# Optimization experiments

Measured on AMD Instinct MI355X. Metric: run time of the kernel, lower is better.

The kernel has to match this reference:

```python
import jax, jax.numpy as jnp
import numpy as np

H = 8          # num_heads
NEG = -1e30    # masked-score value
EPS = 1e-5


def layer_norm(h, g, b):
    mu = jnp.mean(h, -1, keepdims=True)
    v = jnp.mean(jnp.square(h - mu), -1, keepdims=True)
    return (h - mu) * jax.lax.rsqrt(v + EPS) * g + b


def mha(q_in, kv_in, in_w, in_b, out_w, out_b, mask):
    # in_w: [3D, D] packed q/k/v projections (PyTorch MultiheadAttention layout)
    D = q_in.shape[-1]
    dh = D // H
    wq, wk, wv = in_w[:D], in_w[D:2 * D], in_w[2 * D:]
    bq, bk, bv = in_b[:D], in_b[D:2 * D], in_b[2 * D:]
    q = (q_in @ wq.T + bq).reshape(q_in.shape[0], q_in.shape[1], H, dh)
    k = (kv_in @ wk.T + bk).reshape(kv_in.shape[0], kv_in.shape[1], H, dh)
    v = (kv_in @ wv.T + bv).reshape(kv_in.shape[0], kv_in.shape[1], H, dh)
    s = jnp.einsum('bqhd,bkhd->bhqk', q, k) / jnp.sqrt(jnp.float32(dh))
    if mask is not None:
        s = s + mask  # [1,1,S,S] additive causal mask
    a = jax.nn.softmax(s, axis=-1)
    o = jnp.einsum('bhqk,bkhd->bqhd', a, v).reshape(q_in.shape[0], q_in.shape[1], D)
    return o @ out_w.T + out_b


def _forward(x, start_query, one_emb, zero_emb,
             sa_in_w, sa_in_b, sa_out_w, sa_out_b,
             ca_in_w, ca_in_b, ca_out_w, ca_out_b,
             lin1_w, lin1_b, lin2_w, lin2_b,
             ln_g, ln_b, cls_w, cls_b, label):
    B, S, D = x.shape
    n = label.shape[0]  # == S
    # Teacher-forced decoder inputs: [start_query, emb(label[0]), ..., emb(label[n-2])]
    tok = jnp.where((label[:-1] > 0.5)[:, None], one_emb[None, :], zero_emb[None, :])  # [n-1, D]
    tgt = jnp.concatenate([start_query[None, :], tok], axis=0)  # [n, D]
    h = jnp.broadcast_to(tgt[None], (B, n, D))
    causal = jnp.tril(jnp.ones((n, n), dtype=bool))
    mask = jnp.where(causal, 0.0, NEG).astype(x.dtype)[None, None]
    L = sa_in_w.shape[0]
    for l in range(L):
        # post-LN TransformerDecoderLayer (PyTorch default, relu FFN)
        sa = mha(h, h, sa_in_w[l], sa_in_b[l], sa_out_w[l], sa_out_b[l], mask)
        h = layer_norm(h + sa, ln_g[l, 0], ln_b[l, 0])
        ca = mha(h, x, ca_in_w[l], ca_in_b[l], ca_out_w[l], ca_out_b[l], None)
        h = layer_norm(h + ca, ln_g[l, 1], ln_b[l, 1])
        ff = jax.nn.relu(h @ lin1_w[l].T + lin1_b[l]) @ lin2_w[l].T + lin2_b[l]
        h = layer_norm(h + ff, ln_g[l, 2], ln_b[l, 2])
    # classifier + sigmoid; output[b, i] == decoder(tf[:1+i])[-1] of the original loop
    return jax.nn.sigmoid(h @ cls_w.T + cls_b)  # [B, n, 1]


def setup_inputs() -> dict:
    key = jax.random.key(0)
    ks = iter(jax.random.split(key, 32))
    B, S, D, FF, L = 8, 1024, 1024, 2048, 6

    def w(shape, s=0.02):
        return jax.random.normal(next(ks), shape, jnp.float32) * s

    return dict(
        x=jax.random.normal(next(ks), (B, S, D), jnp.float32),
        label=jax.random.uniform(next(ks), (S,), jnp.float32),
        start_query=jax.random.uniform(next(ks), (D,), jnp.float32),
        one_emb=jax.random.uniform(next(ks), (D,), jnp.float32),
        zero_emb=jax.random.uniform(next(ks), (D,), jnp.float32),
        sa_in_w=w((L, 3 * D, D)), sa_in_b=jnp.zeros((L, 3 * D), jnp.float32),
        sa_out_w=w((L, D, D)), sa_out_b=jnp.zeros((L, D), jnp.float32),
        ca_in_w=w((L, 3 * D, D)), ca_in_b=jnp.zeros((L, 3 * D), jnp.float32),
        ca_out_w=w((L, D, D)), ca_out_b=jnp.zeros((L, D), jnp.float32),
        lin1_w=w((L, FF, D)), lin1_b=jnp.zeros((L, FF), jnp.float32),
        lin2_w=w((L, D, FF)), lin2_b=jnp.zeros((L, D), jnp.float32),
        ln_g=jnp.ones((L, 3, D), jnp.float32), ln_b=jnp.zeros((L, 3, D), jnp.float32),
        cls_w=w((1, D)), cls_b=jnp.zeros((1,), jnp.float32),
    )


def reference(x, label, start_query, one_emb, zero_emb,
              sa_in_w, sa_in_b, sa_out_w, sa_out_b,
              ca_in_w, ca_in_b, ca_out_w, ca_out_b,
              lin1_w, lin1_b, lin2_w, lin2_b,
              ln_g, ln_b, cls_w, cls_b):
    return _forward(x, start_query, one_emb, zero_emb,
                    sa_in_w, sa_in_b, sa_out_w, sa_out_b,
                    ca_in_w, ca_in_b, ca_out_w, ca_out_b,
                    lin1_w, lin1_b, lin2_w, lin2_b,
                    ln_g, ln_b, cls_w, cls_b, label)
```

## Files before the change

kernel.cpp:

```cpp
#include <hip/hip_runtime.h>
#include <stdint.h>

typedef __attribute__((ext_vector_type(8))) short short8;
typedef __attribute__((ext_vector_type(4))) float f32x4;
typedef __attribute__((ext_vector_type(4))) float float4v;
typedef __attribute__((ext_vector_type(4))) unsigned short ushort4v;

__device__ __forceinline__ float b2f(short u) {
  union { float f; uint32_t i; } v; v.i = ((uint32_t)(unsigned short)u) << 16; return v.f;
}
__device__ __forceinline__ short f2b(float f) {
  uint32_t x = __float_as_uint(f);
  uint32_t r = (x + 0x7fffu + ((x >> 16) & 1u)) >> 16;
  return (short)r;
}
__device__ __forceinline__ void gload16(const short* g, short* l) {
  __builtin_amdgcn_global_load_lds((__attribute__((address_space(1))) const void*)g,
                                   (__attribute__((address_space(3))) void*)l, 16, 0, 0);
}

__global__ void f2b_kernel(const float* __restrict__ in, short* __restrict__ out, int n4) {
  int i = blockIdx.x * blockDim.x + threadIdx.x;
  int stride = gridDim.x * blockDim.x;
  for (; i < n4; i += stride) {
// ... 25 lines not shown
  const int w3 = w & 3;
  const int rlo = lane >> 3;
  const int us = (lane & 7) ^ rlo;
#pragma unroll
  for (int q = 0; q < 4; ++q) {
    int c;
    if (w < 4) c = g2 * 8 + w3 * 2 + (q & 1) + (q >> 1) * 16;
    else       c = g2 * 4 + w3 + (q & 1) * 8 + (q >> 1) * 16;
    int rih = (c & 15) * 8 + rlo;
    gload16(mat + (rc0 + (c >> 4) * 128 + rih) * (size_t)K + kt * 64 + us * 8,
            dstbuf + ((w >> 2) * 32 + c) * 512);
  }
}

template <int EPI>
__global__ __launch_bounds__(512, 2) void gemm256(const short* __restrict__ A,
                                                  const short* __restrict__ W,
                                                  const float* __restrict__ bias,
                                                  short* __restrict__ C,
                                                  int M, int N, int K) {
  __shared__ short lds[2 * 4 * 8192];
  const int tid = threadIdx.x, lane = tid & 63, w = tid >> 6;
  const int g = lane >> 4, l15 = lane & 15;
  const int wm = w >> 2, wn = w & 3;
  const int nbx = N >> 8;
  int nwg = gridDim.x, orig = blockIdx.x, cpx = nwg >> 3;
  int id = (orig & 7) * cpx + (orig >> 3);
  int bx = id % nbx, by = id / nbx;
  const size_t rowA = (size_t)by * 256, colB = (size_t)bx * 256;
  const int NT = K >> 6;

  const short* smat = (w < 4) ? A : W;
  const size_t src0 = (w < 4) ? rowA : colB;

  f32x4 acc[8][4];
#pragma unroll
  for (int i = 0; i < 8; ++i)
#pragma unroll
    for (int j = 0; j < 4; ++j) acc[i][j] = (f32x4){0.f, 0.f, 0.f, 0.f};

  int sxz0 = g ^ (l15 & 7);
  int sxz1 = (4 + g) ^ (l15 & 7);
  const short* abase = lds + wm * 8192 + l15 * 64;
  const short* bbase = lds + (2 + (wn >> 1)) * 8192 + ((wn & 1) * 64 + l15) * 64;

  stage_grp(smat, src0, K, 0, lds, w, lane, 0);
  stage_grp(smat, src0, K, 0, lds, w, lane, 1);
  asm volatile("s_waitcnt vmcnt(0)" ::: "memory");
  __builtin_amdgcn_s_barrier();

  int p = 0;
  for (int t = 0; t < NT; ++t) {
    const int po = p * 32768;
    short* nbuf = lds + (p ^ 1) * 32768;
    if (t + 1 < NT) stage_grp(smat, src0, K, t + 1, nbuf, w, lane, 0);
    short8 af[4][2], bf0[2][2], bf1[2][2];

#pragma unroll
    for (int i = 0; i < 4; ++i) {
      af[i][0] = *(const short8*)(abase + po + i * 1024 + sxz0 * 8);
      af[i][1] = *(const short8*)(abase + po + i * 1024 + sxz1 * 8);
    }
#pragma unroll
    for (int j = 0; j < 2; ++j) {
      bf0[j][0] = *(const short8*)(bbase + po + j * 1024 + sxz0 * 8);
      bf0[j][1] = *(const short8*)(bbase + po + j * 1024 + sxz1 * 8);
    }
    __builtin_amdgcn_s_barrier();
    __builtin_amdgcn_s_setprio(1);
#pragma unroll
    for (int i = 0; i < 4; ++i)
#pragma unroll
      for (int j = 0; j < 2; ++j)
#pragma unroll
        for (int ks = 0; ks < 2; ++ks)
          acc[i][j] = __builtin_amdgcn_mfma_f32_16x16x32_bf16(af[i][ks], bf0[j][ks], acc[i][j], 0, 0, 0);
    __builtin_amdgcn_s_setprio(0);
    if (t + 1 < NT) {
      asm volatile("s_waitcnt vmcnt(4)" ::: "memory");
      stage_grp(smat, src0, K, t + 1, nbuf, w, lane, 1);
    } else {
      asm volatile("s_waitcnt vmcnt(0)" ::: "memory");
    }
    __builtin_amdgcn_s_barrier();

#pragma unroll
    for (int j = 0; j < 2; ++j) {
      bf1[j][0] = *(const short8*)(bbase + po + (2 + j) * 1024 + sxz0 * 8);
      bf1[j][1] = *(const short8*)(bbase + po + (2 + j) * 1024 + sxz1 * 8);
    }
    __builtin_amdgcn_s_barrier();
    __builtin_amdgcn_s_setprio(1);
#pragma unroll
    for (int i = 0; i < 4; ++i)
#pragma unroll
      for (int j = 0; j < 2; ++j)
#pragma unroll
        for (int ks = 0; ks < 2; ++ks)
          acc[i][2 + j] = __builtin_amdgcn_mfma_f32_16x16x32_bf16(af[i][ks], bf1[j][ks], acc[i][2 + j], 0, 0, 0);
    __builtin_amdgcn_s_setprio(0);
    __builtin_amdgcn_s_barrier();

#pragma unroll
    for (int i = 0; i < 4; ++i) {
      af[i][0] = *(const short8*)(abase + po + (64 + i * 16) * 64 + sxz0 * 8);
      af[i][1] = *(const short8*)(abase + po + (64 + i * 16) * 64 + sxz1 * 8);
    }
    __builtin_amdgcn_s_barrier();
    __builtin_amdgcn_s_setprio(1);
#pragma unroll
    for (int i = 0; i < 4; ++i)
#pragma unroll
      for (int j = 0; j < 2; ++j)
#pragma unroll
        for (int ks = 0; ks < 2; ++ks)
          acc[4 + i][2 + j] = __builtin_amdgcn_mfma_f32_16x16x32_bf16(af[i][ks], bf1[j][ks], acc[4 + i][2 + j], 0, 0, 0);
    __builtin_amdgcn_s_setprio(0);
    __builtin_amdgcn_s_barrier();

    __builtin_amdgcn_s_setprio(1);
#pragma unroll
    for (int i = 0; i < 4; ++i)
#pragma unroll
      for (int j = 0; j < 2; ++j)
#pragma unroll
        for (int ks = 0; ks < 2; ++ks)
          acc[4 + i][j] = __builtin_amdgcn_mfma_f32_16x16x32_bf16(af[i][ks], bf0[j][ks], acc[4 + i][j], 0, 0, 0);
    __builtin_amdgcn_s_setprio(0);

    asm volatile("s_waitcnt vmcnt(4)" ::: "memory");
    __builtin_amdgcn_s_barrier();
    p ^= 1;
  }

  float bv[4];
#pragma unroll
  for (int j = 0; j < 4; ++j) bv[j] = bias[colB + wn * 64 + j * 16 + l15];
#pragma unroll
  for (int i = 0; i < 8; ++i) {
    size_t row = rowA + wm * 128 + i * 16 + g * 4;
#pragma unroll
    for (int j = 0; j < 4; ++j) {
      size_t col = colB + wn * 64 + j * 16 + l15;
#pragma unroll
      for (int r = 0; r < 4; ++r) {
        float v = acc[i][j][r] + bv[j];
        if (EPI == 1) v = fmaxf(v, 0.f);
        C[(row + r) * N + col] = f2b(v);
      }
    }
  }
}

__device__ __forceinline__ void stage_n128(const short* __restrict__ A, const short* __restrict__ W,
                                           size_t rowA, size_t colB, int K, int kt,
                                           short* dstbuf, int w, int lane, int grp) {
  const int rlo = lane >> 3;
  const int us = (lane & 7) ^ rlo;
  const int coff = kt * 64 + us * 8;
  if (grp == 0) {
#pragma unroll
    for (int q = 0; q < 4; ++q) {
      int c = w * 4 + q;
      gload16(A + (rowA + (c >> 4) * 128 + (c & 15) * 8 + rlo) * (size_t)K + coff,
              dstbuf + (c >> 4) * 8192 + (c & 15) * 512 + lane * 8);
    }
    int bc = (w & 3) + (w >> 2) * 8;
    gload16(W + (colB + bc * 8 + rlo) * (size_t)K + coff, dstbuf + 16384 + bc * 512 + lane * 8);
  } else {
    int bc = (w & 3) + (w >> 2) * 8 + 4;
    gload16(W + (colB + bc * 8 + rlo) * (size_t)K + coff, dstbuf + 16384 + bc * 512 + lane * 8);
  }
}

template <int EPI>
__global__ __launch_bounds__(512, 2) void gemm_n128(const short* __restrict__ A,
                                                    const short* __restrict__ W,
                                                    const float* __restrict__ bias,
                                                    short* __restrict__ C,
                                                    int M, int N, int K) {
  __shared__ short lds[2 * 24576];
  const int tid = threadIdx.x, lane = tid & 63, w = tid >> 6;
  const int g = lane >> 4, l15 = lane & 15;
  const int wm = w >> 1, wn = w & 1;
  const int nbx = N >> 7;
  int nwg = gridDim.x, orig = blockIdx.x, cpx = nwg >> 3;
  int id = (orig & 7) * cpx + (orig >> 3);
  int bx = id % nbx, by = id / nbx;
  const size_t rowA = (size_t)by * 256, colB = (size_t)bx * 128;
  const int NT = K >> 6;

  f32x4 acc[4][4];
#pragma unroll
  for (int i = 0; i < 4; ++i)
#pragma unroll
    for (int j = 0; j < 4; ++j) acc[i][j] = (f32x4){0.f, 0.f, 0.f, 0.f};

  const int sxz0 = g ^ (l15 & 7), sxz1 = (4 + g) ^ (l15 & 7);
  int aoff[4];
#pragma unroll
  for (int i = 0; i < 4; ++i) {
    int ra = wm * 64 + i * 16 + l15;
    aoff[i] = (ra >> 7) * 8192 + (ra & 127) * 64;
  }
  const int boffb = 16384 + (wn * 64 + l15) * 64;

  stage_n128(A, W, rowA, colB, K, 0, lds, w, lane, 0);
  stage_n128(A, W, rowA, colB, K, 0, lds, w, lane, 1);
  asm volatile("s_waitcnt vmcnt(0)" ::: "memory");
  __builtin_amdgcn_s_barrier();

  int p = 0;
  for (int t = 0; t < NT; ++t) {
    short* nbuf = lds + (p ^ 1) * 24576;
    if (t + 1 < NT) stage_n128(A, W, rowA, colB, K, t + 1, nbuf, w, lane, 0);
    const int po = p * 24576;
    short8 af[4][2], bf[2][2];
#pragma unroll
    for (int i = 0; i < 4; ++i) {
      af[i][0] = *(const short8*)(lds + po + aoff[i] + sxz0 * 8);
      af[i][1] = *(const short8*)(lds + po + aoff[i] + sxz1 * 8);
    }
#pragma unroll
    for (int j = 0; j < 2; ++j) {
      bf[j][0] = *(const short8*)(lds + po + boffb + j * 1024 + sxz0 * 8);
      bf[j][1] = *(const short8*)(lds + po + boffb + j * 1024 + sxz1 * 8);
    }
    __builtin_amdgcn_s_setprio(1);
#pragma unroll
    for (int i = 0; i < 4; ++i)
#pragma unroll
      for (int j = 0; j < 2; ++j)
#pragma unroll
        for (int ks = 0; ks < 2; ++ks)
          acc[i][j] = __builtin_amdgcn_mfma_f32_16x16x32_bf16(af[i][ks], bf[j][ks], acc[i][j], 0, 0, 0);
    __builtin_amdgcn_s_setprio(0);
    if (t + 1 < NT) {
      asm volatile("s_waitcnt vmcnt(5)" ::: "memory");
      stage_n128(A, W, rowA, colB, K, t + 1, nbuf, w, lane, 1);
    } else {
      asm volatile("s_waitcnt vmcnt(0)" ::: "memory");
    }
    __builtin_amdgcn_s_barrier();
#pragma unroll
    for (int j = 0; j < 2; ++j) {
      bf[j][0] = *(const short8*)(lds + po + boffb + 2048 + j * 1024 + sxz0 * 8);
      bf[j][1] = *(const short8*)(lds + po + boffb + 2048 + j * 1024 + sxz1 * 8);
    }
    __builtin_amdgcn_s_setprio(1);
#pragma unroll
    for (int i = 0; i < 4; ++i)
#pragma unroll
      for (int j = 0; j < 2; ++j)
#pragma unroll
        for (int ks = 0; ks < 2; ++ks)
          acc[i][2 + j] = __builtin_amdgcn_mfma_f32_16x16x32_bf16(af[i][ks], bf[j][ks], acc[i][2 + j], 0, 0, 0);
    __builtin_amdgcn_s_setprio(0);
    asm volatile("s_waitcnt vmcnt(1)" ::: "memory");
    __builtin_amdgcn_s_barrier();
    p ^= 1;
  }

  float bv[4];
#pragma unroll
  for (int j = 0; j < 4; ++j) bv[j] = bias[colB + wn * 64 + j * 16 + l15];
#pragma unroll
  for (int i = 0; i < 4; ++i) {
    size_t row = rowA + wm * 64 + i * 16 + g * 4;
#pragma unroll
    for (int j = 0; j < 4; ++j) {
      size_t col = colB + wn * 64 + j * 16 + l15;
#pragma unroll
      for (int r = 0; r < 4; ++r) {
        float v = acc[i][j][r] + bv[j];
        if (EPI == 1) v = fmaxf(v, 0.f);
        C[(row + r) * N + col] = f2b(v);
      }
    }
  }
}

__global__ __launch_bounds__(256) void tv_kernel(const short* __restrict__ src, int ld, int voff,
                                                 short* __restrict__ vt) {
  __shared__ short t[64 * 72];
  const int kt = blockIdx.x * 64, dt = blockIdx.y * 64, bh = blockIdx.z;
  const int b = bh >> 3, hh = bh & 7;
  const short* s = src + (size_t)(b * 1024 + kt) * ld + voff + hh * 128 + dt;
#pragma unroll
  for (int p = 0; p < 2; ++p) {
    int idx = p * 256 + threadIdx.x;
    int r = idx >> 3, u = idx & 7;
    *(short8*)&t[r * 72 + u * 8] = *(const short8*)&s[(size_t)r * ld + u * 8];
  }
  __syncthreads();
#pragma unroll
  for (int p = 0; p < 2; ++p) {
    int idx = p * 256 + threadIdx.x;
    int dd = idx >> 3, u = idx & 7;
    short8 o;
#pragma unroll
    for (int j = 0; j < 8; ++j) o[j] = t[(u * 8 + j) * 72 + dd];
    *(short8*)&vt[((size_t)bh * 128 + dt + dd) * 1024 + kt + u * 8] = o;
  }
}

template <bool CAUSAL>
__global__ __launch_bounds__(256, 2) void attn_kernel(const short* __restrict__ Qb, int ldq, int qoff,
                                                      const short* __restrict__ Kb, int ldk, int koff,
                                                      const short* __restrict__ Vt,
                                                      short* __restrict__ Ob) {
  __shared__ short k_lds[64 * 128];
  __shared__ short v_lds[128 * 64];
  __shared__ short p_lds[4 * 32 * 72];
  const int tid = threadIdx.x, lane = tid & 63, w = tid >> 6;
  const int g = lane >> 4, l15 = lane & 15;
  const int bh = blockIdx.y, b = bh >> 3, hh = bh & 7;
  int qi = blockIdx.x;
  if (CAUSAL) qi = (blockIdx.y & 32) ? 7 - qi : qi;
  const int q0 = qi * 128;
  const float scale = 0.08838834764831845f;
  const int ntiles = CAUSAL ? (q0 >> 6) + 2 : 16;

  const int kr = (w * 4) * 4 + (lane >> 4);
  const int vd = (w * 4) * 8 + (lane >> 3);

  short8 qf[2][4];
#pragma unroll
  for (int fm = 0; fm < 2; ++fm) {
    int row = q0 + w * 32 + fm * 16 + l15;
    const short* qp = Qb + (size_t)(b * 1024 + row) * ldq + qoff + hh * 128;
#pragma unroll
    for (int t = 0; t < 4; ++t) qf[fm][t] = *(const short8*)(qp + t * 32 + g * 8);
  }

  f32x4 oacc[2][8];
  f32x4 lacc[2];
  float m_st[2][4];
#pragma unroll
  for (int fm = 0; fm < 2; ++fm) {
#pragma unroll
    for (int fo = 0; fo < 8; ++fo) oacc[fm][fo] = (f32x4){0.f, 0.f, 0.f, 0.f};
    lacc[fm] = (f32x4){0.f, 0.f, 0.f, 0.f};
#pragma unroll
    for (int r = 0; r < 4; ++r) m_st[fm][r] = -3.0e38f;
  }
  const short8 ones = {16256, 16256, 16256, 16256, 16256, 16256, 16256, 16256};

#pragma unroll
  for (int c = 0; c < 4; ++c) {
    int ch = w * 4 + c;
    int r = kr + c * 4;
    int us = (lane & 15) ^ (r & 7);
    gload16(Kb + (size_t)(b * 1024 + r) * ldk + koff + hh * 128 + us * 8, k_lds + ch * 512);
    int d = vd + c * 8;
    int usv = (lane & 7) ^ (d & 7);
    gload16(Vt + ((size_t)bh * 128 + d) * 1024 + usv * 8, v_lds + ch * 512);
  }
  __builtin_amdgcn_sched_barrier(0);
  short8 kreg[4], vreg[4];
  if (ntiles > 1) {
#pragma unroll
    for (int c = 0; c < 4; ++c) {
      int r = kr + c * 4;
      int us = (lane & 15) ^ (r & 7);
      kreg[c] = *(const short8*)(Kb + (size_t)(b * 1024 + 64 + r) * ldk + koff + hh * 128 + us * 8);
      int d = vd + c * 8;
      int usv = (lane & 7) ^ (d & 7);
      vreg[c] = *(const short8*)(Vt + ((size_t)bh * 128 + d) * 1024 + 64 + usv * 8);
    }
    asm volatile("s_waitcnt vmcnt(8)" ::: "memory");
  } else {
    asm volatile("s_waitcnt vmcnt(0)" ::: "memory");
  }
  __builtin_amdgcn_s_barrier();

  for (int kt = 0; kt < ntiles; ++kt) {
    f32x4 sacc[2][4];
#pragma unroll
    for (int fm = 0; fm < 2; ++fm)
#pragma unroll
      for (int fn = 0; fn < 4; ++fn) sacc[fm][fn] = (f32x4){0.f, 0.f, 0.f, 0.f};
#pragma unroll
    for (int t = 0; t < 4; ++t) {
      short8 kf[4];
#pragma unroll
      for (int fn = 0; fn < 4; ++fn) {
        int rowk = fn * 16 + l15;
        int u = (4 * t + g) ^ (rowk & 7);
        kf[fn] = *(const short8*)((const char*)k_lds + rowk * 256 + u * 16);
      }
      __builtin_amdgcn_s_setprio(1);
#pragma unroll
      for (int fm = 0; fm < 2; ++fm)
#pragma unroll
        for (int fn = 0; fn < 4; ++fn)
          sacc[fm][fn] = __builtin_amdgcn_mfma_f32_16x16x32_bf16(qf[fm][t], kf[fn], sacc[fm][fn], 0, 0, 0);
      __builtin_amdgcn_s_setprio(0);
    }

#pragma unroll
    for (int fm = 0; fm < 2; ++fm)
#pragma unroll
      for (int reg = 0; reg < 4; ++reg) {
        float sv[4];
        float mt = -3.0e38f;
#pragma unroll
        for (int fn = 0; fn < 4; ++fn) {
          float s = sacc[fm][fn][reg] * scale;
          if (CAUSAL) {
            int kg = kt * 64 + fn * 16 + l15;
            int qg = q0 + w * 32 + fm * 16 + g * 4 + reg;
            if (kg > qg) s = -1e30f;
          }
          sv[fn] = s;
          mt = fmaxf(mt, s);
        }
#pragma unroll
        for (int off = 1; off < 16; off <<= 1) mt = fmaxf(mt, __shfl_xor(mt, off));
        float mo = m_st[fm][reg];
        float mn = fmaxf(mo, mt);
        float corr = __expf(mo - mn);
#pragma unroll
        for (int fn = 0; fn < 4; ++fn) {
          float p = __expf(sv[fn] - mn);
          p_lds[w * 2304 + (fm * 16 + g * 4 + reg) * 72 + fn * 16 + l15] = f2b(p);
        }
        m_st[fm][reg] = mn;
        lacc[fm][reg] *= corr;
#pragma unroll
        for (int fo = 0; fo < 8; ++fo) oacc[fm][fo][reg] *= corr;
      }

#pragma unroll
    for (int t = 0; t < 2; ++t) {
      short8 pf[2];
#pragma unroll
      for (int fm = 0; fm < 2; ++fm)
        pf[fm] = *(const short8*)(p_lds + w * 2304 + (fm * 16 + l15) * 72 + t * 32 + g * 8);
      __builtin_amdgcn_s_setprio(1);
      lacc[0] = __builtin_amdgcn_mfma_f32_16x16x32_bf16(pf[0], ones, lacc[0], 0, 0, 0);
      lacc[1] = __builtin_amdgcn_mfma_f32_16x16x32_bf16(pf[1], ones, lacc[1], 0, 0, 0);
      __builtin_amdgcn_s_setprio(0);
#pragma unroll
      for (int fo = 0; fo < 8; ++fo) {
        int rowd = fo * 16 + l15;
        int u = (4 * t + g) ^ (rowd & 7);
        short8 vf = *(const short8*)((const char*)v_lds + rowd * 128 + u * 16);
        __builtin_amdgcn_s_setprio(1);
#pragma unroll
        for (int fm = 0; fm < 2; ++fm)
          oacc[fm][fo] = __builtin_amdgcn_mfma_f32_16x16x32_bf16(pf[fm], vf, oacc[fm][fo], 0, 0, 0);
        __builtin_amdgcn_s_setprio(0);
      }
    }

    if (kt + 1 < ntiles) {
      __builtin_amdgcn_s_barrier();
      asm volatile("s_waitcnt vmcnt(0)" ::: "memory");
#pragma unroll
      for (int c = 0; c < 4; ++c) {
        int ch = w * 4 + c;
        *(short8*)(k_lds + ch * 512 + lane * 8) = kreg[c];
        *(short8*)(v_lds + ch * 512 + lane * 8) = vreg[c];
      }
      if (kt + 2 < ntiles) {
#pragma unroll
        for (int c = 0; c < 4; ++c) {
          int r = kr + c * 4;
          int us = (lane & 15) ^ (r & 7);
          kreg[c] = *(const short8*)(Kb + (size_t)(b * 1024 + (kt + 2) * 64 + r) * ldk + koff + hh * 128 + us * 8);
          int d = vd + c * 8;
          int usv = (lane & 7) ^ (d & 7);
          vreg[c] = *(const short8*)(Vt + ((size_t)bh * 128 + d) * 1024 + (kt + 2) * 64 + usv * 8);
        }
      }
      asm volatile("s_waitcnt lgkmcnt(0)" ::: "memory");
      __builtin_amdgcn_s_barrier();
    }
  }

#pragma unroll
  for (int fm = 0; fm < 2; ++fm)
#pragma unroll
    for (int fo = 0; fo < 8; ++fo)
#pragma unroll
      for (int reg = 0; reg < 4; ++reg) {
        int row = q0 + w * 32 + fm * 16 + g * 4 + reg;
        int col = hh * 128 + fo * 16 + l15;
        float o = oacc[fm][fo][reg] / lacc[fm][reg];
        Ob[(size_t)(b * 1024 + row) * 1024 + col] = f2b(o);
      }
}

__global__ __launch_bounds__(128) void ln_kernel(const short* __restrict__ h,
                                                 const short* __restrict__ delta,
                                                 const float* __restrict__ gg,
                                                 const float* __restrict__ bb,
                                                 short* __restrict__ out) {
  __shared__ float red[4];
  const int row = blockIdx.x, tid = threadIdx.x;
  const short8 hv = *(const short8*)(h + (size_t)row * 1024 + tid * 8);
  const short8 dv = *(const short8*)(delta + (size_t)row * 1024 + tid * 8);
  float x[8];
  float s = 0.f, s2 = 0.f;
#pragma unroll
  for (int j = 0; j < 8; ++j) {
    x[j] = b2f(hv[j]) + b2f(dv[j]);
    s += x[j];
    s2 += x[j] * x[j];
  }
#pragma unroll
  for (int o = 1; o < 64; o <<= 1) { s += __shfl_xor(s, o); s2 += __shfl_xor(s2, o); }
  if ((tid & 63) == 0) { red[(tid >> 6) * 2] = s; red[(tid >> 6) * 2 + 1] = s2; }
  __syncthreads();
  s = red[0] + red[2];
  s2 = red[1] + red[3];
  const float mu = s * (1.f / 1024.f);
  const float var = s2 * (1.f / 1024.f) - mu * mu;
  const float rs = rsqrtf(var + 1e-5f);
  short8 o;
#pragma unroll
  for (int j = 0; j < 8; ++j) {
    int d = tid * 8 + j;
    o[j] = f2b((x[j] - mu) * rs * gg[d] + bb[d]);
  }
  *(short8*)(out + (size_t)row * 1024 + tid * 8) = o;
}

__global__ __launch_bounds__(256) void cls_kernel(const short* __restrict__ h,
                                                  const float* __restrict__ wv,
                                                  const float* __restrict__ bias,
                                                  float* __restrict__ out) {
  const int lane = threadIdx.x & 63, w = threadIdx.x >> 6;
  const int row = blockIdx.x * 4 + w;
  const short* hp = h + (size_t)row * 1024 + lane * 16;
  float sum = 0.f;
#pragma unroll
  for (int i = 0; i < 2; ++i) {
    short8 v = *(const short8*)(hp + i * 8);
#pragma unroll
    for (int j = 0; j < 8; ++j) sum += b2f(v[j]) * wv[lane * 16 + i * 8 + j];
  }
#pragma unroll
  for (int o = 1; o < 64; o <<= 1) sum += __shfl_xor(sum, o);
  if (lane == 0) {
    float z = sum + bias[0];
    out[row] = 1.f / (1.f + __expf(-z));
  }
}

#define O_SA_IN  ((size_t)0)
#define O_SA_OUT ((size_t)18874368)
#define O_CA_IN  ((size_t)25165824)
#define O_CA_OUT ((size_t)44040192)
#define O_LIN1   ((size_t)50331648)
#define O_LIN2   ((size_t)62914560)
#define O_X      ((size_t)75497472)
#define O_H      ((size_t)83886080)
#define O_QKV    ((size_t)92274688)
#define O_ATTN   ((size_t)117440512)
#define O_DELTA  ((size_t)125829120)
#define O_VT     ((size_t)134217728)
#define O_FF1    ((size_t)142606336)

extern "C" void kernel_launch(void* const* d_in, const int* in_sizes, int n_in,
                              void* d_out, int out_size, void* d_ws, size_t ws_size,
                              hipStream_t stream) {
  const float* x = (const float*)d_in[0];
  const float* label = (const float*)d_in[1];
  const float* sq = (const float*)d_in[2];
  const float* onee = (const float*)d_in[3];
  const float* zeroe = (const float*)d_in[4];
  const float* sa_in_w = (const float*)d_in[5];
  const float* sa_in_b = (const float*)d_in[6];
  const float* sa_out_w = (const float*)d_in[7];
  const float* sa_out_b = (const float*)d_in[8];
  const float* ca_in_w = (const float*)d_in[9];
  const float* ca_in_b = (const float*)d_in[10];
  const float* ca_out_w = (const float*)d_in[11];
  const float* ca_out_b = (const float*)d_in[12];
  const float* lin1_w = (const float*)d_in[13];
  const float* lin1_b = (const float*)d_in[14];
  const float* lin2_w = (const float*)d_in[15];
  const float* lin2_b = (const float*)d_in[16];
  const float* ln_g = (const float*)d_in[17];
  const float* ln_b = (const float*)d_in[18];
  const float* cls_w = (const float*)d_in[19];
  const float* cls_b = (const float*)d_in[20];

  short* ws = (short*)d_ws;
  short* w_sa_in = ws + O_SA_IN;
  short* w_sa_out = ws + O_SA_OUT;
  short* w_ca_in = ws + O_CA_IN;
  short* w_ca_out = ws + O_CA_OUT;
  short* w_lin1 = ws + O_LIN1;
  short* w_lin2 = ws + O_LIN2;
  short* xb = ws + O_X;
  short* hbuf = ws + O_H;
  short* qkv = ws + O_QKV;
  short* kvb = qkv + 8388608;
  short* attnb = ws + O_ATTN;
  short* delta = ws + O_DELTA;
  short* vt = ws + O_VT;
  short* ff1 = ws + O_FF1;

  f2b_kernel<<<4096, 256, 0, stream>>>(sa_in_w, w_sa_in, 18874368 / 4);
  f2b_kernel<<<4096, 256, 0, stream>>>(sa_out_w, w_sa_out, 6291456 / 4);
  f2b_kernel<<<4096, 256, 0, stream>>>(ca_in_w, w_ca_in, 18874368 / 4);
  f2b_kernel<<<4096, 256, 0, stream>>>(ca_out_w, w_ca_out, 6291456 / 4);
  f2b_kernel<<<4096, 256, 0, stream>>>(lin1_w, w_lin1, 12582912 / 4);
  f2b_kernel<<<4096, 256, 0, stream>>>(lin2_w, w_lin2, 12582912 / 4);
  f2b_kernel<<<4096, 256, 0, stream>>>(x, xb, 8388608 / 4);
  h0_kernel<<<1024, 256, 0, stream>>>(label, sq, onee, zeroe, hbuf);

  for (int l = 0; l < 6; ++l) {
    gemm256<0><<<384, 512, 0, stream>>>(hbuf, w_sa_in + (size_t)l * 3145728,
                                        sa_in_b + (size_t)l * 3072, qkv, 8192, 3072, 1024);
    tv_kernel<<<dim3(16, 2, 64), 256, 0, stream>>>(qkv, 3072, 2048, vt);
    attn_kernel<true><<<dim3(8, 64), 256, 0, stream>>>(qkv, 3072, 0, qkv, 3072, 1024, vt, attnb);
    gemm_n128<0><<<256, 512, 0, stream>>>(attnb, w_sa_out + (size_t)l * 1048576,
                                          sa_out_b + (size_t)l * 1024, delta, 8192, 1024, 1024);
    ln_kernel<<<8192, 128, 0, stream>>>(hbuf, delta, ln_g + (size_t)(l * 3 + 0) * 1024,
                                        ln_b + (size_t)(l * 3 + 0) * 1024, hbuf);
    gemm_n128<0><<<256, 512, 0, stream>>>(hbuf, w_ca_in + (size_t)l * 3145728,
                                          ca_in_b + (size_t)l * 3072, qkv, 8192, 1024, 1024);
    gemm256<0><<<256, 512, 0, stream>>>(xb, w_ca_in + (size_t)l * 3145728 + 1048576,
                                        ca_in_b + (size_t)l * 3072 + 1024, kvb, 8192, 2048, 1024);
    tv_kernel<<<dim3(16, 2, 64), 256, 0, stream>>>(kvb, 2048, 1024, vt);
    attn_kernel<false><<<dim3(8, 64), 256, 0, stream>>>(qkv, 1024, 0, kvb, 2048, 0, vt, attnb);
    gemm_n128<0><<<256, 512, 0, stream>>>(attnb, w_ca_out + (size_t)l * 1048576,
                                          ca_out_b + (size_t)l * 1024, delta, 8192, 1024, 1024);
    ln_kernel<<<8192, 128, 0, stream>>>(hbuf, delta, ln_g + (size_t)(l * 3 + 1) * 1024,
                                        ln_b + (size_t)(l * 3 + 1) * 1024, hbuf);
    gemm256<1><<<256, 512, 0, stream>>>(hbuf, w_lin1 + (size_t)l * 2097152,
                                        lin1_b + (size_t)l * 2048, ff1, 8192, 2048, 1024);
    gemm_n128<0><<<256, 512, 0, stream>>>(ff1, w_lin2 + (size_t)l * 2097152,
                                          lin2_b + (size_t)l * 1024, delta, 8192, 1024, 2048);
    ln_kernel<<<8192, 128, 0, stream>>>(hbuf, delta, ln_g + (size_t)(l * 3 + 2) * 1024,
                                        ln_b + (size_t)(l * 3 + 2) * 1024, hbuf);
  }
  cls_kernel<<<2048, 256, 0, stream>>>(hbuf, cls_w, cls_b, (float*)d_out);
}
```

Baseline: 2.680 ms.

## Shrink GEMM and attention tiles, add lazy softmax rescaling

The N=1024 GEMMs now use 128x128 tiles with 256-thread blocks instead of 256x128 with 512 threads, doubling the grid to 512 blocks. The attention kernel now gives each block 64 query rows instead of 128 (one 16-row fragment per wave), doubles its grid, shrinks the P staging buffer and raises the occupancy hint to 3. The online softmax now rescales the running max and accumulators only when a row's new max exceeds the old one by more than 8, skipping most correction multiplies. Together these aim to fill the CUs better and cut exp/rescale work, at the cost of less data reuse per tile and more K/V reloads across blocks.

```diff
diff --git a/kernel.cpp b/kernel.cpp
--- a/kernel.cpp
+++ b/kernel.cpp
@@ -201,9 +201,9 @@
   }
 }
 
-__device__ __forceinline__ void stage_n128(const short* __restrict__ A, const short* __restrict__ W,
-                                           size_t rowA, size_t colB, int K, int kt,
-                                           short* dstbuf, int w, int lane, int grp) {
+__device__ __forceinline__ void stage128(const short* __restrict__ A, const short* __restrict__ W,
+                                         size_t rowA, size_t colB, int K, int kt,
+                                         short* dstbuf, int w, int lane, int grp) {
   const int rlo = lane >> 3;
   const int us = (lane & 7) ^ rlo;
   const int coff = kt * 64 + us * 8;
@@ -211,24 +211,31 @@
 #pragma unroll
     for (int q = 0; q < 4; ++q) {
       int c = w * 4 + q;
-      gload16(A + (rowA + (c >> 4) * 128 + (c & 15) * 8 + rlo) * (size_t)K + coff,
-              dstbuf + (c >> 4) * 8192 + (c & 15) * 512 + lane * 8);
-    }
-    int bc = (w & 3) + (w >> 2) * 8;
-    gload16(W + (colB + bc * 8 + rlo) * (size_t)K + coff, dstbuf + 16384 + bc * 512 + lane * 8);
+      gload16(A + (rowA + c * 8 + rlo) * (size_t)K + coff, dstbuf + c * 512 + lane * 8);
+    }
+#pragma unroll
+    for (int e = 0; e < 2; ++e) {
+      int i8 = w * 2 + e;
+      int bc = (i8 & 3) + ((i8 >> 2) << 3);
+      gload16(W + (colB + bc * 8 + rlo) * (size_t)K + coff, dstbuf + 8192 + bc * 512 + lane * 8);
+    }
   } else {
-    int bc = (w & 3) + (w >> 2) * 8 + 4;
-    gload16(W + (colB + bc * 8 + rlo) * (size_t)K + coff, dstbuf + 16384 + bc * 512 + lane * 8);
+#pragma unroll
+    for (int e = 0; e < 2; ++e) {
+      int i8 = w * 2 + e;
+      int bc = (i8 & 3) + 4 + ((i8 >> 2) << 3);
+      gload16(W + (colB + bc * 8 + rlo) * (size_t)K + coff, dstbuf + 8192 + bc * 512 + lane * 8);
+    }
   }
 }
 
 template <int EPI>
-__global__ __launch_bounds__(512, 2) void gemm_n128(const short* __restrict__ A,
-                                                    const short* __restrict__ W,
-                                                    const float* __restrict__ bias,
-                                                    short* __restrict__ C,
-                                                    int M, int N, int K) {
-  __shared__ short lds[2 * 24576];
+__global__ __launch_bounds__(256, 2) void gemm128(const short* __restrict__ A,
+                                                  const short* __restrict__ W,
+                                                  const float* __restrict__ bias,
+                                                  short* __restrict__ C,
+                                                  int M, int N, int K) {
+  __shared__ short lds[2 * 16384];
   const int tid = threadIdx.x, lane = tid & 63, w = tid >> 6;
   const int g = lane >> 4, l15 = lane & 15;
   const int wm = w >> 1, wn = w & 1;
@@ -236,7 +243,7 @@
   int nwg = gridDim.x, orig = blockIdx.x, cpx = nwg >> 3;
   int id = (orig & 7) * cpx + (orig >> 3);
   int bx = id % nbx, by = id / nbx;
-  const size_t rowA = (size_t)by * 256, colB = (size_t)bx * 128;
+  const size_t rowA = (size_t)by * 128, colB = (size_t)bx * 128;
   const int NT = K >> 6;
 
   f32x4 acc[4][4];
@@ -246,34 +253,29 @@
     for (int j = 0; j < 4; ++j) acc[i][j] = (f32x4){0.f, 0.f, 0.f, 0.f};
 
   const int sxz0 = g ^ (l15 & 7), sxz1 = (4 + g) ^ (l15 & 7);
-  int aoff[4];
-#pragma unroll
-  for (int i = 0; i < 4; ++i) {
-    int ra = wm * 64 + i * 16 + l15;
-    aoff[i] = (ra >> 7) * 8192 + (ra & 127) * 64;
-  }
-  const int boffb = 16384 + (wn * 64 + l15) * 64;
-
-  stage_n128(A, W, rowA, colB, K, 0, lds, w, lane, 0);
-  stage_n128(A, W, rowA, colB, K, 0, lds, w, lane, 1);
+
+  stage128(A, W, rowA, colB, K, 0, lds, w, lane, 0);
+  stage128(A, W, rowA, colB, K, 0, lds, w, lane, 1);
   asm volatile("s_waitcnt vmcnt(0)" ::: "memory");
   __builtin_amdgcn_s_barrier();
 
   int p = 0;
   for (int t = 0; t < NT; ++t) {
-    short* nbuf = lds + (p ^ 1) * 24576;
-    if (t + 1 < NT) stage_n128(A, W, rowA, colB, K, t + 1, nbuf, w, lane, 0);
-    const int po = p * 24576;
+    short* nbuf = lds + (p ^ 1) * 16384;
+    if (t + 1 < NT) stage128(A, W, rowA, colB, K, t + 1, nbuf, w, lane, 0);
+    const int po = p * 16384;
     short8 af[4][2], bf[2][2];
 #pragma unroll
     for (int i = 0; i < 4; ++i) {
-      af[i][0] = *(const short8*)(lds + po + aoff[i] + sxz0 * 8);
-      af[i][1] = *(const short8*)(lds + po + aoff[i] + sxz1 * 8);
+      int ra = wm * 64 + i * 16 + l15;
+      af[i][0] = *(const short8*)(lds + po + ra * 64 + sxz0 * 8);
+      af[i][1] = *(const short8*)(lds + po + ra * 64 + sxz1 * 8);
     }
 #pragma unroll
     for (int j = 0; j < 2; ++j) {
-      bf[j][0] = *(const short8*)(lds + po + boffb + j * 1024 + sxz0 * 8);
-      bf[j][1] = *(const short8*)(lds + po + boffb + j * 1024 + sxz1 * 8);
+      int rb = wn * 64 + j * 16 + l15;
+      bf[j][0] = *(const short8*)(lds + po + 8192 + rb * 64 + sxz0 * 8);
+      bf[j][1] = *(const short8*)(lds + po + 8192 + rb * 64 + sxz1 * 8);
     }
     __builtin_amdgcn_s_setprio(1);
 #pragma unroll
@@ -285,16 +287,17 @@
           acc[i][j] = __builtin_amdgcn_mfma_f32_16x16x32_bf16(af[i][ks], bf[j][ks], acc[i][j], 0, 0, 0);
     __builtin_amdgcn_s_setprio(0);
     if (t + 1 < NT) {
-      asm volatile("s_waitcnt vmcnt(5)" ::: "memory");
-      stage_n128(A, W, rowA, colB, K, t + 1, nbuf, w, lane, 1);
+      asm volatile("s_waitcnt vmcnt(6)" ::: "memory");
+      stage128(A, W, rowA, colB, K, t + 1, nbuf, w, lane, 1);
     } else {
       asm volatile("s_waitcnt vmcnt(0)" ::: "memory");
     }
     __builtin_amdgcn_s_barrier();
 #pragma unroll
     for (int j = 0; j < 2; ++j) {
-      bf[j][0] = *(const short8*)(lds + po + boffb + 2048 + j * 1024 + sxz0 * 8);
-      bf[j][1] = *(const short8*)(lds + po + boffb + 2048 + j * 1024 + sxz1 * 8);
+      int rb = wn * 64 + 32 + j * 16 + l15;
+      bf[j][0] = *(const short8*)(lds + po + 8192 + rb * 64 + sxz0 * 8);
+      bf[j][1] = *(const short8*)(lds + po + 8192 + rb * 64 + sxz1 * 8);
     }
     __builtin_amdgcn_s_setprio(1);
 #pragma unroll
@@ -305,7 +308,7 @@
         for (int ks = 0; ks < 2; ++ks)
           acc[i][2 + j] = __builtin_amdgcn_mfma_f32_16x16x32_bf16(af[i][ks], bf[j][ks], acc[i][2 + j], 0, 0, 0);
     __builtin_amdgcn_s_setprio(0);
-    asm volatile("s_waitcnt vmcnt(1)" ::: "memory");
+    asm volatile("s_waitcnt vmcnt(2)" ::: "memory");
     __builtin_amdgcn_s_barrier();
     p ^= 1;
   }
@@ -354,45 +357,40 @@
 }
 
 template <bool CAUSAL>
-__global__ __launch_bounds__(256, 2) void attn_kernel(const short* __restrict__ Qb, int ldq, int qoff,
+__global__ __launch_bounds__(256, 3) void attn_kernel(const short* __restrict__ Qb, int ldq, int qoff,
                                                       const short* __restrict__ Kb, int ldk, int koff,
                                                       const short* __restrict__ Vt,
                                                       short* __restrict__ Ob) {
   __shared__ short k_lds[64 * 128];
   __shared__ short v_lds[128 * 64];
-  __shared__ short p_lds[4 * 32 * 72];
+  __shared__ short p_lds[4 * 16 * 72];
   const int tid = threadIdx.x, lane = tid & 63, w = tid >> 6;
   const int g = lane >> 4, l15 = lane & 15;
   const int bh = blockIdx.y, b = bh >> 3, hh = bh & 7;
   int qi = blockIdx.x;
-  if (CAUSAL) qi = (blockIdx.y & 32) ? 7 - qi : qi;
-  const int q0 = qi * 128;
+  if (CAUSAL) qi = (blockIdx.y & 32) ? 15 - qi : qi;
+  const int q0 = qi * 64;
   const float scale = 0.08838834764831845f;
-  const int ntiles = CAUSAL ? (q0 >> 6) + 2 : 16;
-
-  const int kr = (w * 4) * 4 + (lane >> 4);
-  const int vd = (w * 4) * 8 + (lane >> 3);
-
-  short8 qf[2][4];
-#pragma unroll
-  for (int fm = 0; fm < 2; ++fm) {
-    int row = q0 + w * 32 + fm * 16 + l15;
+  const int ntiles = CAUSAL ? qi + 1 : 16;
+
+  const int kr = w * 16 + (lane >> 4);
+  const int vd = w * 32 + (lane >> 3);
+
+  short8 qf[4];
+  {
+    int row = q0 + w * 16 + l15;
     const short* qp = Qb + (size_t)(b * 1024 + row) * ldq + qoff + hh * 128;
 #pragma unroll
-    for (int t = 0; t < 4; ++t) qf[fm][t] = *(const short8*)(qp + t * 32 + g * 8);
-  }
-
-  f32x4 oacc[2][8];
-  f32x4 lacc[2];
-  float m_st[2][4];
-#pragma unroll
-  for (int fm = 0; fm < 2; ++fm) {
-#pragma unroll
-    for (int fo = 0; fo < 8; ++fo) oacc[fm][fo] = (f32x4){0.f, 0.f, 0.f, 0.f};
-    lacc[fm] = (f32x4){0.f, 0.f, 0.f, 0.f};
-#pragma unroll
-    for (int r = 0; r < 4; ++r) m_st[fm][r] = -3.0e38f;
-  }
+    for (int t = 0; t < 4; ++t) qf[t] = *(const short8*)(qp + t * 32 + g * 8);
+  }
+
+  f32x4 oacc[8];
+  f32x4 lacc = (f32x4){0.f, 0.f, 0.f, 0.f};
+  float m_st[4];
+#pragma unroll
+  for (int fo = 0; fo < 8; ++fo) oacc[fo] = (f32x4){0.f, 0.f, 0.f, 0.f};
+#pragma unroll
+  for (int r = 0; r < 4; ++r) m_st[r] = -3.0e38f;
   const short8 ones = {16256, 16256, 16256, 16256, 16256, 16256, 16256, 16256};
 
 #pragma unroll
@@ -424,11 +422,9 @@
   __builtin_amdgcn_s_barrier();
 
   for (int kt = 0; kt < ntiles; ++kt) {
-    f32x4 sacc[2][4];
-#pragma unroll
-    for (int fm = 0; fm < 2; ++fm)
-#pragma unroll
-      for (int fn = 0; fn < 4; ++fn) sacc[fm][fn] = (f32x4){0.f, 0.f, 0.f, 0.f};
+    f32x4 sacc[4];
+#pragma unroll
+    for (int fn = 0; fn < 4; ++fn) sacc[fn] = (f32x4){0.f, 0.f, 0.f, 0.f};
 #pragma unroll
     for (int t = 0; t < 4; ++t) {
       short8 kf[4];
@@ -440,55 +436,50 @@
       }
       __builtin_amdgcn_s_setprio(1);
 #pragma unroll
-      for (int fm = 0; fm < 2; ++fm)
-#pragma unroll
-        for (int fn = 0; fn < 4; ++fn)
-          sacc[fm][fn] = __builtin_amdgcn_mfma_f32_16x16x32_bf16(qf[fm][t], kf[fn], sacc[fm][fn], 0, 0, 0);
+      for (int fn = 0; fn < 4; ++fn)
+        sacc[fn] = __builtin_amdgcn_mfma_f32_16x16x32_bf16(qf[t], kf[fn], sacc[fn], 0, 0, 0);
       __builtin_amdgcn_s_setprio(0);
     }
 
 #pragma unroll
-    for (int fm = 0; fm < 2; ++fm)
-#pragma unroll
-      for (int reg = 0; reg < 4; ++reg) {
-        float sv[4];
-        float mt = -3.0e38f;
-#pragma unroll
-        for (int fn = 0; fn < 4; ++fn) {
-          float s = sacc[fm][fn][reg] * scale;
-          if (CAUSAL) {
-            int kg = kt * 64 + fn * 16 + l15;
-            int qg = q0 + w * 32 + fm * 16 + g * 4 + reg;
-            if (kg > qg) s = -1e30f;
-          }
-          sv[fn] = s;
-          mt = fmaxf(mt, s);
+    for (int reg = 0; reg < 4; ++reg) {
+      float sv[4];
+      float mt = -3.0e38f;
+#pragma unroll
+      for (int fn = 0; fn < 4; ++fn) {
+        float s = sacc[fn][reg] * scale;
+        if (CAUSAL) {
+          int kg = kt * 64 + fn * 16 + l15;
+          int qg = q0 + w * 16 + g * 4 + reg;
+          if (kg > qg) s = -1e30f;
         }
-#pragma unroll
-        for (int off = 1; off < 16; off <<= 1) mt = fmaxf(mt, __shfl_xor(mt, off));
-        float mo = m_st[fm][reg];
+        sv[fn] = s;
+        mt = fmaxf(mt, s);
+      }
+#pragma unroll
+      for (int off = 1; off < 16; off <<= 1) mt = fmaxf(mt, __shfl_xor(mt, off));
+      float mo = m_st[reg];
+      if (__any(mt > mo + 8.f)) {
         float mn = fmaxf(mo, mt);
         float corr = __expf(mo - mn);
-#pragma unroll
-        for (int fn = 0; fn < 4; ++fn) {
-          float p = __expf(sv[fn] - mn);
-          p_lds[w * 2304 + (fm * 16 + g * 4 + reg) * 72 + fn * 16 + l15] = f2b(p);
-        }
-        m_st[fm][reg] = mn;
-        lacc[fm][reg] *= corr;
-#pragma unroll
-        for (int fo = 0; fo < 8; ++fo) oacc[fm][fo][reg] *= corr;
-      }
+        lacc[reg] *= corr;
+#pragma unroll
+        for (int fo = 0; fo < 8; ++fo) oacc[fo][reg] *= corr;
+        m_st[reg] = mn;
+        mo = mn;
+      }
+#pragma unroll
+      for (int fn = 0; fn < 4; ++fn) {
+        float p = __expf(sv[fn] - mo);
+        p_lds[w * 1152 + (g * 4 + reg) * 72 + fn * 16 + l15] = f2b(p);
+      }
+    }
 
 #pragma unroll
     for (int t = 0; t < 2; ++t) {
-      short8 pf[2];
-#pragma unroll
-      for (int fm = 0; fm < 2; ++fm)
-        pf[fm] = *(const short8*)(p_lds + w * 2304 + (fm * 16 + l15) * 72 + t * 32 + g * 8);
+      short8 pf = *(const short8*)(p_lds + w * 1152 + l15 * 72 + t * 32 + g * 8);
       __builtin_amdgcn_s_setprio(1);
-      lacc[0] = __builtin_amdgcn_mfma_f32_16x16x32_bf16(pf[0], ones, lacc[0], 0, 0, 0);
-      lacc[1] = __builtin_amdgcn_mfma_f32_16x16x32_bf16(pf[1], ones, lacc[1], 0, 0, 0);
+      lacc = __builtin_amdgcn_mfma_f32_16x16x32_bf16(pf, ones, lacc, 0, 0, 0);
       __builtin_amdgcn_s_setprio(0);
 #pragma unroll
       for (int fo = 0; fo < 8; ++fo) {
@@ -496,9 +487,7 @@
         int u = (4 * t + g) ^ (rowd & 7);
         short8 vf = *(const short8*)((const char*)v_lds + rowd * 128 + u * 16);
         __builtin_amdgcn_s_setprio(1);
-#pragma unroll
-        for (int fm = 0; fm < 2; ++fm)
-          oacc[fm][fo] = __builtin_amdgcn_mfma_f32_16x16x32_bf16(pf[fm], vf, oacc[fm][fo], 0, 0, 0);
+        oacc[fo] = __builtin_amdgcn_mfma_f32_16x16x32_bf16(pf, vf, oacc[fo], 0, 0, 0);
         __builtin_amdgcn_s_setprio(0);
       }
     }
@@ -529,16 +518,14 @@
   }
 
 #pragma unroll
-  for (int fm = 0; fm < 2; ++fm)
-#pragma unroll
-    for (int fo = 0; fo < 8; ++fo)
-#pragma unroll
-      for (int reg = 0; reg < 4; ++reg) {
-        int row = q0 + w * 32 + fm * 16 + g * 4 + reg;
-        int col = hh * 128 + fo * 16 + l15;
-        float o = oacc[fm][fo][reg] / lacc[fm][reg];
-        Ob[(size_t)(b * 1024 + row) * 1024 + col] = f2b(o);
-      }
+  for (int fo = 0; fo < 8; ++fo)
+#pragma unroll
+    for (int reg = 0; reg < 4; ++reg) {
+      int row = q0 + w * 16 + g * 4 + reg;
+      int col = hh * 128 + fo * 16 + l15;
+      float o = oacc[fo][reg] / lacc[reg];
+      Ob[(size_t)(b * 1024 + row) * 1024 + col] = f2b(o);
+    }
 }
 
 __global__ __launch_bounds__(128) void ln_kernel(const short* __restrict__ h,
@@ -666,25 +653,25 @@
     gemm256<0><<<384, 512, 0, stream>>>(hbuf, w_sa_in + (size_t)l * 3145728,
                                         sa_in_b + (size_t)l * 3072, qkv, 8192, 3072, 1024);
     tv_kernel<<<dim3(16, 2, 64), 256, 0, stream>>>(qkv, 3072, 2048, vt);
-    attn_kernel<true><<<dim3(8, 64), 256, 0, stream>>>(qkv, 3072, 0, qkv, 3072, 1024, vt, attnb);
-    gemm_n128<0><<<256, 512, 0, stream>>>(attnb, w_sa_out + (size_t)l * 1048576,
-                                          sa_out_b + (size_t)l * 1024, delta, 8192, 1024, 1024);
+    attn_kernel<true><<<dim3(16, 64), 256, 0, stream>>>(qkv, 3072, 0, qkv, 3072, 1024, vt, attnb);
+    gemm128<0><<<512, 256, 0, stream>>>(attnb, w_sa_out + (size_t)l * 1048576,
+                                        sa_out_b + (size_t)l * 1024, delta, 8192, 1024, 1024);
     ln_kernel<<<8192, 128, 0, stream>>>(hbuf, delta, ln_g + (size_t)(l * 3 + 0) * 1024,
                                         ln_b + (size_t)(l * 3 + 0) * 1024, hbuf);
-    gemm_n128<0><<<256, 512, 0, stream>>>(hbuf, w_ca_in + (size_t)l * 3145728,
-                                          ca_in_b + (size_t)l * 3072, qkv, 8192, 1024, 1024);
+    gemm128<0><<<512, 256, 0, stream>>>(hbuf, w_ca_in + (size_t)l * 3145728,
+                                        ca_in_b + (size_t)l * 3072, qkv, 8192, 1024, 1024);
     gemm256<0><<<256, 512, 0, stream>>>(xb, w_ca_in + (size_t)l * 3145728 + 1048576,
                                         ca_in_b + (size_t)l * 3072 + 1024, kvb, 8192, 2048, 1024);
     tv_kernel<<<dim3(16, 2, 64), 256, 0, stream>>>(kvb, 2048, 1024, vt);
-    attn_kernel<false><<<dim3(8, 64), 256, 0, stream>>>(qkv, 1024, 0, kvb, 2048, 0, vt, attnb);
-    gemm_n128<0><<<256, 512, 0, stream>>>(attnb, w_ca_out + (size_t)l * 1048576,
-                                          ca_out_b + (size_t)l * 1024, delta, 8192, 1024, 1024);
+    attn_kernel<false><<<dim3(16, 64), 256, 0, stream>>>(qkv, 1024, 0, kvb, 2048, 0, vt, attnb);
+    gemm128<0><<<512, 256, 0, stream>>>(attnb, w_ca_out + (size_t)l * 1048576,
+                                        ca_out_b + (size_t)l * 1024, delta, 8192, 1024, 1024);
     ln_kernel<<<8192, 128, 0, stream>>>(hbuf, delta, ln_g + (size_t)(l * 3 + 1) * 1024,
                                         ln_b + (size_t)(l * 3 + 1) * 1024, hbuf);
     gemm256<1><<<256, 512, 0, stream>>>(hbuf, w_lin1 + (size_t)l * 2097152,
                                         lin1_b + (size_t)l * 2048, ff1, 8192, 2048, 1024);
-    gemm_n128<0><<<256, 512, 0, stream>>>(ff1, w_lin2 + (size_t)l * 2097152,
-                                          lin2_b + (size_t)l * 1024, delta, 8192, 1024, 2048);
+    gemm128<0><<<512, 256, 0, stream>>>(ff1, w_lin2 + (size_t)l * 2097152,
+                                        lin2_b + (size_t)l * 1024, delta, 8192, 1024, 2048);
     ln_kernel<<<8192, 128, 0, stream>>>(hbuf, delta, ln_g + (size_t)(l * 3 + 2) * 1024,
                                         ln_b + (size_t)(l * 3 + 2) * 1024, hbuf);
   }
```

New measurement: 4.100 ms. +53.0%, slower.

## Shrink N=1024 GEMM tile to 128x128 with 256 threads and reorder attention grid

Applied to the files above, without the earlier changes.

The N=1024 projection GEMMs switch from a 256x128 tile with 512 threads to a 128x128 tile with 256 threads. This doubles the workgroup count to 512 so the CUs are filled better, and it rebalances the load staging and vmcnt waits to match. The attention launch grid is transposed so the batch-head index is on x and the query tile on y, which drops the causal reversal trick used for load balancing. The smaller tile lowers operand reuse per workgroup, and the causal attention may now schedule less evenly.

```diff
diff --git a/kernel.cpp b/kernel.cpp
--- a/kernel.cpp
+++ b/kernel.cpp
@@ -201,9 +201,9 @@
   }
 }
 
-__device__ __forceinline__ void stage_n128(const short* __restrict__ A, const short* __restrict__ W,
-                                           size_t rowA, size_t colB, int K, int kt,
-                                           short* dstbuf, int w, int lane, int grp) {
+__device__ __forceinline__ void stage128(const short* __restrict__ A, const short* __restrict__ W,
+                                         size_t rowA, size_t colB, int K, int kt,
+                                         short* dstbuf, int w, int lane, int grp) {
   const int rlo = lane >> 3;
   const int us = (lane & 7) ^ rlo;
   const int coff = kt * 64 + us * 8;
@@ -211,24 +211,31 @@
 #pragma unroll
     for (int q = 0; q < 4; ++q) {
       int c = w * 4 + q;
-      gload16(A + (rowA + (c >> 4) * 128 + (c & 15) * 8 + rlo) * (size_t)K + coff,
-              dstbuf + (c >> 4) * 8192 + (c & 15) * 512 + lane * 8);
-    }
-    int bc = (w & 3) + (w >> 2) * 8;
-    gload16(W + (colB + bc * 8 + rlo) * (size_t)K + coff, dstbuf + 16384 + bc * 512 + lane * 8);
+      gload16(A + (rowA + c * 8 + rlo) * (size_t)K + coff, dstbuf + c * 512 + lane * 8);
+    }
+#pragma unroll
+    for (int e = 0; e < 2; ++e) {
+      int i8 = w * 2 + e;
+      int bc = (i8 & 3) + ((i8 >> 2) << 3);
+      gload16(W + (colB + bc * 8 + rlo) * (size_t)K + coff, dstbuf + 8192 + bc * 512 + lane * 8);
+    }
   } else {
-    int bc = (w & 3) + (w >> 2) * 8 + 4;
-    gload16(W + (colB + bc * 8 + rlo) * (size_t)K + coff, dstbuf + 16384 + bc * 512 + lane * 8);
+#pragma unroll
+    for (int e = 0; e < 2; ++e) {
+      int i8 = w * 2 + e;
+      int bc = (i8 & 3) + 4 + ((i8 >> 2) << 3);
+      gload16(W + (colB + bc * 8 + rlo) * (size_t)K + coff, dstbuf + 8192 + bc * 512 + lane * 8);
+    }
   }
 }
 
 template <int EPI>
-__global__ __launch_bounds__(512, 2) void gemm_n128(const short* __restrict__ A,
-                                                    const short* __restrict__ W,
-                                                    const float* __restrict__ bias,
-                                                    short* __restrict__ C,
-                                                    int M, int N, int K) {
-  __shared__ short lds[2 * 24576];
+__global__ __launch_bounds__(256, 2) void gemm128(const short* __restrict__ A,
+                                                  const short* __restrict__ W,
+                                                  const float* __restrict__ bias,
+                                                  short* __restrict__ C,
+                                                  int M, int N, int K) {
+  __shared__ short lds[2 * 16384];
   const int tid = threadIdx.x, lane = tid & 63, w = tid >> 6;
   const int g = lane >> 4, l15 = lane & 15;
   const int wm = w >> 1, wn = w & 1;
@@ -236,7 +243,7 @@
   int nwg = gridDim.x, orig = blockIdx.x, cpx = nwg >> 3;
   int id = (orig & 7) * cpx + (orig >> 3);
   int bx = id % nbx, by = id / nbx;
-  const size_t rowA = (size_t)by * 256, colB = (size_t)bx * 128;
+  const size_t rowA = (size_t)by * 128, colB = (size_t)bx * 128;
   const int NT = K >> 6;
 
   f32x4 acc[4][4];
@@ -246,34 +253,29 @@
     for (int j = 0; j < 4; ++j) acc[i][j] = (f32x4){0.f, 0.f, 0.f, 0.f};
 
   const int sxz0 = g ^ (l15 & 7), sxz1 = (4 + g) ^ (l15 & 7);
-  int aoff[4];
-#pragma unroll
-  for (int i = 0; i < 4; ++i) {
-    int ra = wm * 64 + i * 16 + l15;
-    aoff[i] = (ra >> 7) * 8192 + (ra & 127) * 64;
-  }
-  const int boffb = 16384 + (wn * 64 + l15) * 64;
-
-  stage_n128(A, W, rowA, colB, K, 0, lds, w, lane, 0);
-  stage_n128(A, W, rowA, colB, K, 0, lds, w, lane, 1);
+
+  stage128(A, W, rowA, colB, K, 0, lds, w, lane, 0);
+  stage128(A, W, rowA, colB, K, 0, lds, w, lane, 1);
   asm volatile("s_waitcnt vmcnt(0)" ::: "memory");
   __builtin_amdgcn_s_barrier();
 
   int p = 0;
   for (int t = 0; t < NT; ++t) {
-    short* nbuf = lds + (p ^ 1) * 24576;
-    if (t + 1 < NT) stage_n128(A, W, rowA, colB, K, t + 1, nbuf, w, lane, 0);
-    const int po = p * 24576;
+    short* nbuf = lds + (p ^ 1) * 16384;
+    if (t + 1 < NT) stage128(A, W, rowA, colB, K, t + 1, nbuf, w, lane, 0);
+    const int po = p * 16384;
     short8 af[4][2], bf[2][2];
 #pragma unroll
     for (int i = 0; i < 4; ++i) {
-      af[i][0] = *(const short8*)(lds + po + aoff[i] + sxz0 * 8);
-      af[i][1] = *(const short8*)(lds + po + aoff[i] + sxz1 * 8);
+      int ra = wm * 64 + i * 16 + l15;
+      af[i][0] = *(const short8*)(lds + po + ra * 64 + sxz0 * 8);
+      af[i][1] = *(const short8*)(lds + po + ra * 64 + sxz1 * 8);
     }
 #pragma unroll
     for (int j = 0; j < 2; ++j) {
-      bf[j][0] = *(const short8*)(lds + po + boffb + j * 1024 + sxz0 * 8);
-      bf[j][1] = *(const short8*)(lds + po + boffb + j * 1024 + sxz1 * 8);
+      int rb = wn * 64 + j * 16 + l15;
+      bf[j][0] = *(const short8*)(lds + po + 8192 + rb * 64 + sxz0 * 8);
+      bf[j][1] = *(const short8*)(lds + po + 8192 + rb * 64 + sxz1 * 8);
     }
     __builtin_amdgcn_s_setprio(1);
 #pragma unroll
@@ -285,16 +287,17 @@
           acc[i][j] = __builtin_amdgcn_mfma_f32_16x16x32_bf16(af[i][ks], bf[j][ks], acc[i][j], 0, 0, 0);
     __builtin_amdgcn_s_setprio(0);
     if (t + 1 < NT) {
-      asm volatile("s_waitcnt vmcnt(5)" ::: "memory");
-      stage_n128(A, W, rowA, colB, K, t + 1, nbuf, w, lane, 1);
+      asm volatile("s_waitcnt vmcnt(6)" ::: "memory");
+      stage128(A, W, rowA, colB, K, t + 1, nbuf, w, lane, 1);
     } else {
       asm volatile("s_waitcnt vmcnt(0)" ::: "memory");
     }
     __builtin_amdgcn_s_barrier();
 #pragma unroll
     for (int j = 0; j < 2; ++j) {
-      bf[j][0] = *(const short8*)(lds + po + boffb + 2048 + j * 1024 + sxz0 * 8);
-      bf[j][1] = *(const short8*)(lds + po + boffb + 2048 + j * 1024 + sxz1 * 8);
+      int rb = wn * 64 + 32 + j * 16 + l15;
+      bf[j][0] = *(const short8*)(lds + po + 8192 + rb * 64 + sxz0 * 8);
+      bf[j][1] = *(const short8*)(lds + po + 8192 + rb * 64 + sxz1 * 8);
     }
     __builtin_amdgcn_s_setprio(1);
 #pragma unroll
@@ -305,7 +308,7 @@
         for (int ks = 0; ks < 2; ++ks)
           acc[i][2 + j] = __builtin_amdgcn_mfma_f32_16x16x32_bf16(af[i][ks], bf[j][ks], acc[i][2 + j], 0, 0, 0);
     __builtin_amdgcn_s_setprio(0);
-    asm volatile("s_waitcnt vmcnt(1)" ::: "memory");
+    asm volatile("s_waitcnt vmcnt(2)" ::: "memory");
     __builtin_amdgcn_s_barrier();
     p ^= 1;
   }
@@ -363,15 +366,14 @@
   __shared__ short p_lds[4 * 32 * 72];
   const int tid = threadIdx.x, lane = tid & 63, w = tid >> 6;
   const int g = lane >> 4, l15 = lane & 15;
-  const int bh = blockIdx.y, b = bh >> 3, hh = bh & 7;
-  int qi = blockIdx.x;
-  if (CAUSAL) qi = (blockIdx.y & 32) ? 7 - qi : qi;
+  const int bh = blockIdx.x, b = bh >> 3, hh = bh & 7;
+  const int qi = blockIdx.y;
   const int q0 = qi * 128;
   const float scale = 0.08838834764831845f;
   const int ntiles = CAUSAL ? (q0 >> 6) + 2 : 16;
 
-  const int kr = (w * 4) * 4 + (lane >> 4);
-  const int vd = (w * 4) * 8 + (lane >> 3);
+  const int kr = w * 16 + (lane >> 4);
+  const int vd = w * 32 + (lane >> 3);
 
   short8 qf[2][4];
 #pragma unroll
@@ -666,25 +668,25 @@
     gemm256<0><<<384, 512, 0, stream>>>(hbuf, w_sa_in + (size_t)l * 3145728,
                                         sa_in_b + (size_t)l * 3072, qkv, 8192, 3072, 1024);
     tv_kernel<<<dim3(16, 2, 64), 256, 0, stream>>>(qkv, 3072, 2048, vt);
-    attn_kernel<true><<<dim3(8, 64), 256, 0, stream>>>(qkv, 3072, 0, qkv, 3072, 1024, vt, attnb);
-    gemm_n128<0><<<256, 512, 0, stream>>>(attnb, w_sa_out + (size_t)l * 1048576,
-                                          sa_out_b + (size_t)l * 1024, delta, 8192, 1024, 1024);
+    attn_kernel<true><<<dim3(64, 8), 256, 0, stream>>>(qkv, 3072, 0, qkv, 3072, 1024, vt, attnb);
+    gemm128<0><<<512, 256, 0, stream>>>(attnb, w_sa_out + (size_t)l * 1048576,
+                                        sa_out_b + (size_t)l * 1024, delta, 8192, 1024, 1024);
     ln_kernel<<<8192, 128, 0, stream>>>(hbuf, delta, ln_g + (size_t)(l * 3 + 0) * 1024,
                                         ln_b + (size_t)(l * 3 + 0) * 1024, hbuf);
-    gemm_n128<0><<<256, 512, 0, stream>>>(hbuf, w_ca_in + (size_t)l * 3145728,
-                                          ca_in_b + (size_t)l * 3072, qkv, 8192, 1024, 1024);
+    gemm128<0><<<512, 256, 0, stream>>>(hbuf, w_ca_in + (size_t)l * 3145728,
+                                        ca_in_b + (size_t)l * 3072, qkv, 8192, 1024, 1024);
     gemm256<0><<<256, 512, 0, stream>>>(xb, w_ca_in + (size_t)l * 3145728 + 1048576,
                                         ca_in_b + (size_t)l * 3072 + 1024, kvb, 8192, 2048, 1024);
     tv_kernel<<<dim3(16, 2, 64), 256, 0, stream>>>(kvb, 2048, 1024, vt);
-    attn_kernel<false><<<dim3(8, 64), 256, 0, stream>>>(qkv, 1024, 0, kvb, 2048, 0, vt, attnb);
-    gemm_n128<0><<<256, 512, 0, stream>>>(attnb, w_ca_out + (size_t)l * 1048576,
-                                          ca_out_b + (size_t)l * 1024, delta, 8192, 1024, 1024);
+    attn_kernel<false><<<dim3(64, 8), 256, 0, stream>>>(qkv, 1024, 0, kvb, 2048, 0, vt, attnb);
+    gemm128<0><<<512, 256, 0, stream>>>(attnb, w_ca_out + (size_t)l * 1048576,
+                                        ca_out_b + (size_t)l * 1024, delta, 8192, 1024, 1024);
     ln_kernel<<<8192, 128, 0, stream>>>(hbuf, delta, ln_g + (size_t)(l * 3 + 1) * 1024,
                                         ln_b + (size_t)(l * 3 + 1) * 1024, hbuf);
     gemm256<1><<<256, 512, 0, stream>>>(hbuf, w_lin1 + (size_t)l * 2097152,
                                         lin1_b + (size_t)l * 2048, ff1, 8192, 2048, 1024);
-    gemm_n128<0><<<256, 512, 0, stream>>>(ff1, w_lin2 + (size_t)l * 2097152,
-                                          lin2_b + (size_t)l * 1024, delta, 8192, 1024, 2048);
+    gemm128<0><<<512, 256, 0, stream>>>(ff1, w_lin2 + (size_t)l * 2097152,
+                                        lin2_b + (size_t)l * 1024, delta, 8192, 1024, 2048);
     ln_kernel<<<8192, 128, 0, stream>>>(hbuf, delta, ln_g + (size_t)(l * 3 + 2) * 1024,
                                         ln_b + (size_t)(l * 3 + 2) * 1024, hbuf);
   }
```

New measurement: 2.570 ms. 4.1% less time.
